# Kernel optimization log

Hardware: AMD Instinct MI355X
Metric: run time of the kernel (lower is better)

## Reference

```python
import jax, jax.numpy as jnp
import numpy as np

L, HID, NH, NKV, HD, INTER = 16, 960, 15, 5, 64, 2560
VOCAB, NV, NT, PRE, SD = 49152, 192, 48, 241, 32
THETA, EPS, B = 100000.0, 1e-5, 16
GROUPS = NH // NKV


def setup_inputs() -> dict:
    key = jax.random.key(0)
    ks = jax.random.split(key, 20)
    s = 0.02
    rn = lambda k, shp: jax.random.normal(k, shp, jnp.float32) * s
    return {
        'vision_features': jax.random.normal(ks[0], (B, NV, HID), jnp.float32),
        'lang_token_ids': jax.random.randint(ks[1], (B, NT), 0, VOCAB),
        'lang_mask': jnp.ones((B, NT), dtype=bool),
        'state': jax.random.normal(ks[2], (B, SD), jnp.float32),
        'embed': rn(ks[3], (VOCAB, HID)),
        'state_w': rn(ks[4], (SD, HID)),
        'state_b': jnp.zeros((HID,), jnp.float32),
        'Wq': rn(ks[5], (L, HID, NH * HD)),
        'Wk': rn(ks[6], (L, HID, NKV * HD)),
        'Wv': rn(ks[7], (L, HID, NKV * HD)),
        'Wo': rn(ks[8], (L, NH * HD, HID)),
        'Wg': rn(ks[9], (L, HID, INTER)),
        'Wu': rn(ks[10], (L, HID, INTER)),
        'Wd': rn(ks[11], (L, INTER, HID)),
        'ln1': jnp.ones((L, HID), jnp.float32),
        'ln2': jnp.ones((L, HID), jnp.float32),
    }


def _rms(x, w):
    var = jnp.mean(jnp.square(x), axis=-1, keepdims=True)
    return x * jax.lax.rsqrt(var + EPS) * w


def _rotate_half(x):
    h = x.shape[-1] // 2
    return jnp.concatenate([-x[..., h:], x[..., :h]], axis=-1)


def _rope_tables(position_ids):
    # position_ids: [B, S] -> cos/sin: [B, S, HD]
    inv_freq = 1.0 / (THETA ** (jnp.arange(0, HD, 2, dtype=jnp.float32) / HD))
    freqs = position_ids.astype(jnp.float32)[..., None] * inv_freq  # [B,S,HD/2]
    emb = jnp.concatenate([freqs, freqs], axis=-1)
    return jnp.cos(emb), jnp.sin(emb)


def _apply_rope(x, cos, sin):
    # x: [B,S,H,D]; cos/sin: [B,S,D]
    return x * cos[:, :, None, :] + _rotate_half(x) * sin[:, :, None, :]


def _attention(q, k, v, mask2d):
    # q: [B,S,NH,HD]; k,v: [B,S,NKV,HD]; mask2d: [B,S,S] bool (query i, key j)
    kx = jnp.repeat(k, GROUPS, axis=2)  # GQA expand -> [B,S,NH,HD]
    vx = jnp.repeat(v, GROUPS, axis=2)
    scores = jnp.einsum('bihd,bjhd->bhij', q, kx) * (HD ** -0.5)
    big_neg = jnp.finfo(jnp.float32).min
    scores = jnp.where(mask2d[:, None, :, :], scores, big_neg)
    probs = jax.nn.softmax(scores, axis=-1)
    out = jnp.einsum('bhij,bjhd->bihd', probs, vx)
    return out.reshape(q.shape[0], q.shape[1], NH * HD)


def reference(vision_features, lang_token_ids, lang_mask, state,
              embed, state_w, state_b, Wq, Wk, Wv, Wo, Wg, Wu, Wd, ln1, ln2):
    lang_emb = embed[lang_token_ids] * jnp.sqrt(jnp.float32(HID))  # [B,NT,HID]
    state_emb = (state @ state_w + state_b)[:, None, :]            # [B,1,HID]
    x = jnp.concatenate([vision_features, lang_emb, state_emb], axis=1)  # [B,PRE,HID]

    pad = jnp.concatenate([jnp.ones((B, NV), bool), lang_mask.astype(bool),
                           jnp.ones((B, 1), bool)], axis=1)  # [B,PRE]
    position_ids = jnp.clip(jnp.cumsum(pad.astype(jnp.int32), axis=1) - 1, 0, None)
    cos, sin = _rope_tables(position_ids)

    att_marks = jnp.zeros((PRE,), jnp.int32).at[NV + NT:].set(1)
    cum = jnp.cumsum(att_marks)
    att2d = cum[None, :] >= cum[:, None]  # [S_q, S_kv]: key cum <= query cum
    pad2d = pad[:, :, None] & pad[:, None, :]
    mask2d = att2d[None, :, :] & pad2d  # [B,S,S]

    def layer(x, w):
        h = _rms(x, w['ln1'])
        S = h.shape[1]
        q = (h @ w['Wq']).reshape(B, S, NH, HD)
        k = (h @ w['Wk']).reshape(B, S, NKV, HD)
        v = (h @ w['Wv']).reshape(B, S, NKV, HD)
        q = _apply_rope(q, cos, sin)
        k = _apply_rope(k, cos, sin)
        a = _attention(q, k, v, mask2d)
        x = x + a @ w['Wo']
        h2 = _rms(x, w['ln2'])
        m = (jax.nn.silu(h2 @ w['Wg']) * (h2 @ w['Wu'])) @ w['Wd']
        return x + m, (k, v)

    weights = {'Wq': Wq, 'Wk': Wk, 'Wv': Wv, 'Wo': Wo,
               'Wg': Wg, 'Wu': Wu, 'Wd': Wd, 'ln1': ln1, 'ln2': ln2}
    _, (keys, values) = jax.lax.scan(layer, x, weights)
    # keys/values: [L, B, PRE, NKV, HD]
    return keys, values
```

## Files before the change

### kernel.cpp

```cpp
#include <hip/hip_runtime.h>
#include <hip/hip_bf16.h>

namespace {

typedef __bf16 bf16_t;
typedef __bf16 bf16x8 __attribute__((ext_vector_type(8)));
typedef __bf16 bf16x4 __attribute__((ext_vector_type(4)));
typedef float f32x4 __attribute__((ext_vector_type(4)));

constexpr int kL     = 16;
constexpr int kHid   = 960;
constexpr int kNH    = 15;
constexpr int kNKV   = 5;
constexpr int kHD    = 64;
constexpr int kInter = 2560;
constexpr int kNV    = 192;
constexpr int kNT    = 48;
constexpr int kPre   = 241;
constexpr int kSD    = 32;
constexpr int kB     = 16;
constexpr int kTok   = kB * kPre;
constexpr int kTokP  = 3968;
constexpr int kQKV   = 1600;
constexpr float kEps = 1e-5f;
constexpr float kSqrtHid = 30.98386677f;

constexpr size_t kWoOff     = (size_t)1664 * 960;
constexpr size_t kWgOff     = kWoOff + (size_t)1024 * 960;
constexpr size_t kWuOff     = kWgOff + (size_t)2560 * 960;
constexpr size_t kWdOff     = kWuOff + (size_t)2560 * 960;
constexpr size_t kWPerLayer = kWdOff + (size_t)1024 * 2560;

__device__ __forceinline__ void gload16(const bf16_t* g, bf16_t* l) {
  __builtin_amdgcn_global_load_lds((const __attribute__((address_space(1))) void*)g,
                                   (__attribute__((address_space(3))) void*)l, 16, 0, 0);
}

__device__ __forceinline__ void xcd_tile(int& bx, int& by) {
  int nbx = gridDim.x;
  int nwg = nbx * gridDim.y;
  int orig = blockIdx.y * nbx + blockIdx.x;
  int q = nwg >> 3, r = nwg & 7;
  int xcd = orig & 7, pos = orig >> 3;
  int swz = (xcd < r) ? (xcd * (q + 1) + pos) : (r * (q + 1) + (xcd - r) * q + pos);
  bx = swz % nbx;
  by = swz / nbx;
}

__global__ void build_x_kernel(const float* __restrict__ vision,
                               const int*   __restrict__ tokens,
                               const float* __restrict__ state,
                               const float* __restrict__ embed,
                               const float* __restrict__ sw,
                               const float* __restrict__ sb,
                               float* __restrict__ x) {
  int idx = blockIdx.x * blockDim.x + threadIdx.x;
  if (idx >= kTok * kHid) return;
  int t = idx / kHid, c = idx - t * kHid;
  int b = t / kPre, s = t - b * kPre;
  float v;
  if (s < kNV) {
    v = vision[((size_t)b * kNV + s) * kHid + c];
  } else if (s < kNV + kNT) {
    int tok = tokens[b * kNT + (s - kNV)];
    v = embed[(size_t)tok * kHid + c] * kSqrtHid;
  } else {
    float acc = sb[c];
#pragma unroll
    for (int i = 0; i < kSD; ++i) acc += state[b * kSD + i] * sw[i * kHid + c];
    v = acc;
  }
  x[idx] = v;
}

__global__ void rope_table_kernel(float* __restrict__ cosT, float* __restrict__ sinT) {
  int idx = blockIdx.x * blockDim.x + threadIdx.x;
  if (idx >= kPre * 32) return;
  int s = idx >> 5, fi = idx & 31;
  float inv = __expf(-(2.0f * (float)fi / (float)kHD) * __logf(100000.0f));
  float fr = (float)s * inv;
  cosT[idx] = cosf(fr);
  sinT[idx] = sinf(fr);
}

__device__ void transpose_tile(const float* __restrict__ src, bf16_t* __restrict__ dst,
                               int K, int N, int tile) {
  __shared__ float ts[64][65];
  int ntn = N >> 6;
  int tk = tile / ntn, tn = tile - tk * ntn;
  int t = threadIdx.x;
  int r = t >> 2, c0 = (t & 3) << 4;
  const float* sp = src + (size_t)((tk << 6) + r) * N + (tn << 6) + c0;
  float4 a = ((const float4*)sp)[0];
  float4 b = ((const float4*)sp)[1];
  float4 c = ((const float4*)sp)[2];
  float4 d = ((const float4*)sp)[3];
  ts[r][c0 + 0] = a.x;  ts[r][c0 + 1] = a.y;  ts[r][c0 + 2] = a.z;  ts[r][c0 + 3] = a.w;
  ts[r][c0 + 4] = b.x;  ts[r][c0 + 5] = b.y;  ts[r][c0 + 6] = b.z;  ts[r][c0 + 7] = b.w;
  ts[r][c0 + 8] = c.x;  ts[r][c0 + 9] = c.y;  ts[r][c0 +10] = c.z;  ts[r][c0 +11] = c.w;
  ts[r][c0 +12] = d.x;  ts[r][c0 +13] = d.y;  ts[r][c0 +14] = d.z;  ts[r][c0 +15] = d.w;
  __syncthreads();
  bf16_t* dp = dst + (size_t)((tn << 6) + r) * K + (tk << 6) + c0;
  bf16x8 o0, o1;
#pragma unroll
  for (int i = 0; i < 8; ++i) o0[i] = (bf16_t)ts[c0 + i][r];
#pragma unroll
  for (int i = 0; i < 8; ++i) o1[i] = (bf16_t)ts[c0 + 8 + i][r];
  *(bf16x8*)dp = o0;
  *(bf16x8*)(dp + 8) = o1;
}

__global__ __launch_bounds__(256)
void wconv_kernel(const float* __restrict__ Wq, const float* __restrict__ Wk,
                  const float* __restrict__ Wv, const float* __restrict__ Wo,
                  const float* __restrict__ Wg, const float* __restrict__ Wu,
                  const float* __restrict__ Wd, bf16_t* __restrict__ wall) {
  int bid = blockIdx.x;
  int l = bid / 2400, t = bid - l * 2400;
  bf16_t* wl = wall + (size_t)l * kWPerLayer;
  if      (t < 225)  transpose_tile(Wq + (size_t)l * 921600, wl, 960, 960, t);
  else if (t < 300)  transpose_tile(Wk + (size_t)l * 307200, wl + (size_t)960 * 960, 960, 320, t - 225);
  else if (t < 375)  transpose_tile(Wv + (size_t)l * 307200, wl + (size_t)1280 * 960, 960, 320, t - 300);
  else if (t < 600)  transpose_tile(Wo + (size_t)l * 921600, wl + kWoOff, 960, 960, t - 375);
  else if (t < 1200) transpose_tile(Wg + (size_t)l * 2457600, wl + kWgOff, 960, 2560, t - 600);
  else if (t < 1800) transpose_tile(Wu + (size_t)l * 2457600, wl + kWuOff, 960, 2560, t - 1200);
  else               transpose_tile(Wd + (size_t)l * 2457600, wl + kWdOff, 2560, 960, t - 1800);
}

__global__ __launch_bounds__(256)
void rmsnorm_bf16_kernel(const float* __restrict__ x, const float* __restrict__ w,
                         bf16_t* __restrict__ h) {
  int wid = threadIdx.x >> 6, lane = threadIdx.x & 63;
  int t = blockIdx.x * 4 + wid;
  if (t >= kTok) return;
  const float* xr = x + (size_t)t * kHid;
  float4 v[4];
  float ss = 0.f;
#pragma unroll
  for (int i = 0; i < 4; ++i) {
    int j = lane + i * 64;
    v[i] = make_float4(0.f, 0.f, 0.f, 0.f);
    if (j < 240) v[i] = ((const float4*)xr)[j];
    ss += v[i].x * v[i].x + v[i].y * v[i].y + v[i].z * v[i].z + v[i].w * v[i].w;
  }
#pragma unroll
  for (int off = 32; off; off >>= 1) ss += __shfl_xor(ss, off);
  float scale = rsqrtf(ss * (1.f / (float)kHid) + kEps);
  bf16_t* hr = h + (size_t)t * kHid;
#pragma unroll
  for (int i = 0; i < 4; ++i) {
    int j = lane + i * 64;
    if (j < 240) {
      float4 wv = ((const float4*)w)[j];
      bf16x4 o;
      o[0] = (bf16_t)(v[i].x * scale * wv.x);
      o[1] = (bf16_t)(v[i].y * scale * wv.y);
      o[2] = (bf16_t)(v[i].z * scale * wv.z);
      o[3] = (bf16_t)(v[i].w * scale * wv.w);
      *(bf16x4*)&hr[j * 4] = o;
    }
  }
}


__global__ __launch_bounds__(256, 4)
void gemm_qkv_kernel(const bf16_t* __restrict__ A, const bf16_t* __restrict__ Bt,
                     bf16_t* __restrict__ qkv, float* __restrict__ outk,
                     float* __restrict__ outv,
                     const float* __restrict__ cosT, const float* __restrict__ sinT) {
  constexpr int K = kHid;
  constexpr int NT = K / 32;
  __shared__ alignas(16) bf16_t As[2][4096];
  __shared__ alignas(16) bf16_t Bs[2][2048];
  int tid = threadIdx.x;
  int bx, by;
  xcd_tile(bx, by);
  int m0 = by * 128, n0 = bx * 64;
  int lane = tid & 63, wid = tid >> 6;
  int wr = wid * 32;
  int r0 = tid >> 2, c0 = (tid & 3) * 8;
  int lr = lane & 15, lg = lane >> 4;

  const bf16_t* a0 = A + (size_t)(m0 + r0) * K + c0;
  const bf16_t* a1 = a0 + (size_t)64 * K;
  const bf16_t* b0 = Bt + (size_t)(n0 + r0) * K + c0;

  f32x4 acc[2][4];
#pragma unroll
  for (int m = 0; m < 2; ++m)
#pragma unroll
    for (int n = 0; n < 4; ++n) acc[m][n] = (f32x4){0.f, 0.f, 0.f, 0.f};

  int arow0 = (wr + lr) * 32 + lg * 8;
  int brow0 = lr * 32 + lg * 8;

  gload16(a0, &As[0][tid * 8]);
  gload16(a1, &As[0][2048 + tid * 8]);
  if (r0 < 64) gload16(b0, &Bs[0][tid * 8]);
  __syncthreads();

  int cur = 0;
  for (int t = 0; t < NT; ++t) {
    if (t + 1 < NT) {
      int k1 = (t + 1) * 32;
      gload16(a0 + k1, &As[cur ^ 1][tid * 8]);
      gload16(a1 + k1, &As[cur ^ 1][2048 + tid * 8]);
      gload16(b0 + k1, &Bs[cur ^ 1][tid * 8]);
    }
    bf16x8 af[2], bfr[4];
#pragma unroll
    for (int m = 0; m < 2; ++m) af[m] = *(const bf16x8*)&As[cur][arow0 + m * 16 * 32];
#pragma unroll
    for (int n = 0; n < 4; ++n) bfr[n] = *(const bf16x8*)&Bs[cur][brow0 + n * 16 * 32];
#pragma unroll
    for (int m = 0; m < 2; ++m)
#pragma unroll
      for (int n = 0; n < 4; ++n)
        acc[m][n] = __builtin_amdgcn_mfma_f32_16x16x32_bf16(af[m], bfr[n], acc[m][n], 0, 0, 0);
    __syncthreads();
    cur ^= 1;
  }

  int cbase = n0;
  int cr4 = lg * 4;
  if (cbase < 1280) {
    bool isQ = cbase < 960;
    float scale = isQ ? 0.125f : 1.0f;
#pragma unroll
    for (int m = 0; m < 2; ++m) {
      int row = m0 + wr + m * 16 + cr4;
#pragma unroll
      for (int r = 0; r < 4; ++r) {
        int rr = row + r;
        if (rr >= kTok) continue;
        int s = rr % kPre;
        bf16_t* qrow = qkv + (size_t)rr * kQKV + cbase;
        float* krow = outk + (size_t)rr * 320 + (cbase - 960);
#pragma unroll
        for (int n = 0; n < 2; ++n) {
          int d = n * 16 + lr;
          float c = cosT[s * 32 + d], sn = sinT[s * 32 + d];
          float lo = acc[m][n][r], hi = acc[m][n + 2][r];
          float y0 = lo * c - hi * sn;
          float y1 = hi * c + lo * sn;
          qrow[d]      = (bf16_t)(y0 * scale);
          qrow[d + 32] = (bf16_t)(y1 * scale);
          if (!isQ) { krow[d] = y0; krow[d + 32] = y1; }
        }
      }
    }
  } else {
#pragma unroll
    for (int m = 0; m < 2; ++m) {
      int row = m0 + wr + m * 16 + cr4;
#pragma unroll
      for (int r = 0; r < 4; ++r) {
        int rr = row + r;
        if (rr >= kTok) continue;
        bf16_t* qrow = qkv + (size_t)rr * kQKV + cbase;
        float* vrow = outv + (size_t)rr * 320 + (cbase - 1280);
#pragma unroll
        for (int n = 0; n < 4; ++n) {
          int d = n * 16 + lr;
          float v = acc[m][n][r];
          qrow[d] = (bf16_t)v;
          vrow[d] = v;
        }
      }
    }
  }
}

__global__ __launch_bounds__(256, 4)
void gemm_res_kernel(const bf16_t* __restrict__ A, const bf16_t* __restrict__ Bt,
                     const float* __restrict__ src, float* __restrict__ C,
                     int M, int N, int K) {
  __shared__ alignas(16) bf16_t As[2][4096];
  __shared__ alignas(16) bf16_t Bs[2][2048];
  int tid = threadIdx.x;
  int bx, by;
  xcd_tile(bx, by);
  int m0 = by * 128, n0 = bx * 64;
  int lane = tid & 63, wid = tid >> 6;
  int wr = wid * 32;
  int r0 = tid >> 2, c0 = (tid & 3) * 8;
  int lr = lane & 15, lg = lane >> 4;

  const bf16_t* a0 = A + (size_t)(m0 + r0) * K + c0;
  const bf16_t* a1 = a0 + (size_t)64 * K;
  const bf16_t* b0 = Bt + (size_t)(n0 + r0) * K + c0;

  f32x4 acc[2][4];
#pragma unroll
  for (int m = 0; m < 2; ++m)
#pragma unroll
    for (int n = 0; n < 4; ++n) acc[m][n] = (f32x4){0.f, 0.f, 0.f, 0.f};

  int arow0 = (wr + lr) * 32 + lg * 8;
  int brow0 = lr * 32 + lg * 8;

  gload16(a0, &As[0][tid * 8]);
  gload16(a1, &As[0][2048 + tid * 8]);
  gload16(b0, &Bs[0][tid * 8]);
  __syncthreads();

  int NT = K / 32;
  int cur = 0;
  for (int t = 0; t < NT; ++t) {
    if (t + 1 < NT) {
      int k1 = (t + 1) * 32;
      gload16(a0 + k1, &As[cur ^ 1][tid * 8]);
      gload16(a1 + k1, &As[cur ^ 1][2048 + tid * 8]);
      gload16(b0 + k1, &Bs[cur ^ 1][tid * 8]);
    }
    bf16x8 af[2], bfr[4];
#pragma unroll
    for (int m = 0; m < 2; ++m) af[m] = *(const bf16x8*)&As[cur][arow0 + m * 16 * 32];
#pragma unroll
    for (int n = 0; n < 4; ++n) bfr[n] = *(const bf16x8*)&Bs[cur][brow0 + n * 16 * 32];
#pragma unroll
    for (int m = 0; m < 2; ++m)
#pragma unroll
      for (int n = 0; n < 4; ++n)
        acc[m][n] = __builtin_amdgcn_mfma_f32_16x16x32_bf16(af[m], bfr[n], acc[m][n], 0, 0, 0);
    __syncthreads();
    cur ^= 1;
  }

  int cr4 = lg * 4;
#pragma unroll
  for (int m = 0; m < 2; ++m) {
    int row = m0 + wr + m * 16 + cr4;
#pragma unroll
    for (int n = 0; n < 4; ++n) {
      int col = n0 + n * 16 + lr;
#pragma unroll
      for (int r = 0; r < 4; ++r) {
        int rr = row + r;
        if (rr < M) {
          size_t off = (size_t)rr * N + col;
          C[off] = src[off] + acc[m][n][r];
        }
      }
    }
  }
}

__global__ __launch_bounds__(256)
void gemm_dual_kernel(const bf16_t* __restrict__ A, const bf16_t* __restrict__ Bg,
                      const bf16_t* __restrict__ Bu, bf16_t* __restrict__ act,
                      int M, int K) {
  __shared__ alignas(16) bf16_t As[2][4096];
  __shared__ alignas(16) bf16_t Gs[2][2048];
  __shared__ alignas(16) bf16_t Us[2][2048];
  int tid = threadIdx.x;
  int bx, by;
  xcd_tile(bx, by);
  int m0 = by * 128, n0 = bx * 64;
  int lane = tid & 63, wid = tid >> 6;
  int wr = wid * 32;
  int r0 = tid >> 2, c0 = (tid & 3) * 8;
  int lr = lane & 15, lg = lane >> 4;

  const bf16_t* a0 = A + (size_t)(m0 + r0) * K + c0;
  const bf16_t* a1 = a0 + (size_t)64 * K;
  const bf16_t* g0 = Bg + (size_t)(n0 + r0) * K + c0;
  const bf16_t* u0 = Bu + (size_t)(n0 + r0) * K + c0;

  f32x4 accg[2][4], accu[2][4];
#pragma unroll
  for (int m = 0; m < 2; ++m)
#pragma unroll
    for (int n = 0; n < 4; ++n) {
      accg[m][n] = (f32x4){0.f, 0.f, 0.f, 0.f};
      accu[m][n] = (f32x4){0.f, 0.f, 0.f, 0.f};
    }

  int arow0 = (wr + lr) * 32 + lg * 8;
  int brow0 = lr * 32 + lg * 8;

  gload16(a0, &As[0][tid * 8]);
  gload16(a1, &As[0][2048 + tid * 8]);
  gload16(g0, &Gs[0][tid * 8]);
  gload16(u0, &Us[0][tid * 8]);
  __syncthreads();

  int NT = K / 32;
  int cur = 0;
  for (int t = 0; t < NT; ++t) {
    if (t + 1 < NT) {
      int k1 = (t + 1) * 32;
      gload16(a0 + k1, &As[cur ^ 1][tid * 8]);
      gload16(a1 + k1, &As[cur ^ 1][2048 + tid * 8]);
      gload16(g0 + k1, &Gs[cur ^ 1][tid * 8]);
      gload16(u0 + k1, &Us[cur ^ 1][tid * 8]);
    }
    bf16x8 af[2], bfr[4];
#pragma unroll
    for (int m = 0; m < 2; ++m) af[m] = *(const bf16x8*)&As[cur][arow0 + m * 16 * 32];
#pragma unroll
    for (int n = 0; n < 4; ++n) bfr[n] = *(const bf16x8*)&Gs[cur][brow0 + n * 16 * 32];
#pragma unroll
    for (int m = 0; m < 2; ++m)
#pragma unroll
      for (int n = 0; n < 4; ++n)
        accg[m][n] = __builtin_amdgcn_mfma_f32_16x16x32_bf16(af[m], bfr[n], accg[m][n], 0, 0, 0);
#pragma unroll
    for (int n = 0; n < 4; ++n) bfr[n] = *(const bf16x8*)&Us[cur][brow0 + n * 16 * 32];
#pragma unroll
    for (int m = 0; m < 2; ++m)
#pragma unroll
      for (int n = 0; n < 4; ++n)
        accu[m][n] = __builtin_amdgcn_mfma_f32_16x16x32_bf16(af[m], bfr[n], accu[m][n], 0, 0, 0);
    __syncthreads();
    cur ^= 1;
  }

  int cr4 = lg * 4;
#pragma unroll
  for (int m = 0; m < 2; ++m) {
    int row = m0 + wr + m * 16 + cr4;
#pragma unroll
    for (int n = 0; n < 4; ++n) {
      int col = n0 + n * 16 + lr;
#pragma unroll
      for (int r = 0; r < 4; ++r) {
        int rr = row + r;
        if (rr < M) {
          float g = accg[m][n][r];
          float u = accu[m][n][r];
          float silu = g / (1.f + __expf(-g));
          act[(size_t)rr * kInter + col] = (bf16_t)(silu * u);
        }
      }
    }
  }
}

__global__ __launch_bounds__(256)
void attn_mfma_kernel(const bf16_t* __restrict__ qkv, bf16_t* __restrict__ aout) {
  int h = blockIdx.x, b = blockIdx.y;
  int kvh = h / 3;
  constexpr int LDK = 72;
  constexpr int LDV = 264;
  __shared__ alignas(16) bf16_t Ks[256 * LDK];
  __shared__ alignas(16) bf16_t Vt[64 * LDV];
  __shared__ alignas(16) bf16_t Ps[4][16 * LDV];
  const bf16_t* base = qkv + (size_t)b * kPre * kQKV;
  int tid = threadIdx.x;
  for (int i = tid; i < 2048; i += 256) {
    int j = i >> 3, c = (i & 7) * 8;
    bf16x8 k8, v8;
    if (j < kPre) {
      k8 = *(const bf16x8*)(base + (size_t)j * kQKV + 960 + kvh * 64 + c);
      v8 = *(const bf16x8*)(base + (size_t)j * kQKV + 1280 + kvh * 64 + c);
    } else {
#pragma unroll
      for (int e = 0; e < 8; ++e) { k8[e] = (bf16_t)0.f; v8[e] = (bf16_t)0.f; }
    }
    *(bf16x8*)&Ks[j * LDK + c] = k8;
#pragma unroll
    for (int e = 0; e < 8; ++e) Vt[(c + e) * LDV + j] = v8[e];
  }
  __syncthreads();
  int wid = tid >> 6, lane = tid & 63;
  int lr = lane & 15, lg = lane >> 4;
  bf16_t* myP = &Ps[wid][0];
  for (int qt = wid * 4; qt < wid * 4 + 4; ++qt) {
    int q0 = qt * 16;
    int qrow = q0 + lr; if (qrow > 240) qrow = 240;
    const bf16_t* qp = base + (size_t)qrow * kQKV + h * 64 + lg * 8;
    bf16x8 aq0 = *(const bf16x8*)qp;
    bf16x8 aq1 = *(const bf16x8*)(qp + 32);
    f32x4 sacc[16];
#pragma unroll
    for (int ct = 0; ct < 16; ++ct) sacc[ct] = (f32x4){0.f, 0.f, 0.f, 0.f};
#pragma unroll
    for (int ct = 0; ct < 16; ++ct) {
      int key = ct * 16 + lr;
      bf16x8 kb0 = *(const bf16x8*)&Ks[key * LDK + lg * 8];
      sacc[ct] = __builtin_amdgcn_mfma_f32_16x16x32_bf16(aq0, kb0, sacc[ct], 0, 0, 0);
      bf16x8 kb1 = *(const bf16x8*)&Ks[key * LDK + 32 + lg * 8];
      sacc[ct] = __builtin_amdgcn_mfma_f32_16x16x32_bf16(aq1, kb1, sacc[ct], 0, 0, 0);
    }
    float rmax[4] = {-1e30f, -1e30f, -1e30f, -1e30f};
#pragma unroll
    for (int ct = 0; ct < 16; ++ct) {
      int j = ct * 16 + lr;
#pragma unroll
      for (int r = 0; r < 4; ++r) {
        int q = q0 + lg * 4 + r;
        bool ok = (q < 240) ? (j < kPre) : (j == 240);
        float s = ok ? sacc[ct][r] : -1e30f;
        sacc[ct][r] = s;
        rmax[r] = fmaxf(rmax[r], s);
      }
    }
#pragma unroll
    for (int off = 8; off; off >>= 1) {
#pragma unroll
      for (int r = 0; r < 4; ++r) rmax[r] = fmaxf(rmax[r], __shfl_xor(rmax[r], off));
    }
    float rsum[4] = {0.f, 0.f, 0.f, 0.f};
#pragma unroll
    for (int ct = 0; ct < 16; ++ct) {
#pragma unroll
      for (int r = 0; r < 4; ++r) {
        float s = sacc[ct][r];
        float e = (s > -1e29f) ? __expf(s - rmax[r]) : 0.f;
        rsum[r] += e;
        myP[(lg * 4 + r) * LDV + ct * 16 + lr] = (bf16_t)e;
      }
    }
#pragma unroll
    for (int off = 8; off; off >>= 1) {
#pragma unroll
      for (int r = 0; r < 4; ++r) rsum[r] += __shfl_xor(rsum[r], off);
    }
    f32x4 oacc[4];
#pragma unroll
    for (int dt = 0; dt < 4; ++dt) oacc[dt] = (f32x4){0.f, 0.f, 0.f, 0.f};
#pragma unroll
    for (int ks = 0; ks < 8; ++ks) {
      bf16x8 pa = *(const bf16x8*)&myP[lr * LDV + ks * 32 + lg * 8];
#pragma unroll
      for (int dt = 0; dt < 4; ++dt) {
        bf16x8 vbf = *(const bf16x8*)&Vt[(dt * 16 + lr) * LDV + ks * 32 + lg * 8];
        oacc[dt] = __builtin_amdgcn_mfma_f32_16x16x32_bf16(pa, vbf, oacc[dt], 0, 0, 0);
      }
    }
    float linv[4];
#pragma unroll
    for (int r = 0; r < 4; ++r) linv[r] = 1.f / rsum[r];
#pragma unroll
    for (int dt = 0; dt < 4; ++dt) {
#pragma unroll
      for (int r = 0; r < 4; ++r) {
        int q = q0 + lg * 4 + r;
        if (q < kPre) {
          aout[((size_t)b * kPre + q) * kHid + h * 64 + dt * 16 + lr] =
              (bf16_t)(oacc[dt][r] * linv[r]);
        }
      }
    }
  }
}

}

extern "C" void kernel_launch(void* const* d_in, const int* in_sizes, int n_in,
                              void* d_out, int out_size, void* d_ws, size_t ws_size,
                              hipStream_t stream) {
  const float* vision = (const float*)d_in[0];
  const int*   tokens = (const int*)d_in[1];
  const float* state = (const float*)d_in[3];
  const float* embed = (const float*)d_in[4];
  const float* sw    = (const float*)d_in[5];
  const float* sb    = (const float*)d_in[6];
  const float* Wq    = (const float*)d_in[7];
  const float* Wk    = (const float*)d_in[8];
  const float* Wv    = (const float*)d_in[9];
  const float* Wo    = (const float*)d_in[10];
  const float* Wg    = (const float*)d_in[11];
  const float* Wu    = (const float*)d_in[12];
  const float* Wd    = (const float*)d_in[13];
  const float* ln1   = (const float*)d_in[14];
  const float* ln2   = (const float*)d_in[15];

  char* w = (char*)d_ws;
  float*  x      = (float*)w;   w += (size_t)kTok * kHid * 4;
  bf16_t* qkv    = (bf16_t*)w;  w += (size_t)kTok * kQKV * 2;
  bf16_t* h_bf   = (bf16_t*)w;  w += (size_t)kTokP * kHid * 2;
  bf16_t* a_bf   = (bf16_t*)w;  w += (size_t)kTokP * kHid * 2;
  bf16_t* act_bf = (bf16_t*)w;  w += (size_t)kTokP * kInter * 2;
  bf16_t* wall   = (bf16_t*)w;  w += kWPerLayer * kL * 2;
  float*  cosT   = (float*)w;   w += (size_t)kPre * 32 * 4;
  float*  sinT   = (float*)w;   w += (size_t)kPre * 32 * 4;

  float* out_k = (float*)d_out;
  float* out_v = out_k + (size_t)kL * kTok * 320;

  build_x_kernel<<<(kTok * kHid + 255) / 256, 256, 0, stream>>>(
      vision, tokens, state, embed, sw, sb, x);
  rope_table_kernel<<<(kPre * 32 + 255) / 256, 256, 0, stream>>>(cosT, sinT);
  wconv_kernel<<<2400 * kL, 256, 0, stream>>>(Wq, Wk, Wv, Wo, Wg, Wu, Wd, wall);

  for (int l = 0; l < kL; ++l) {
    bf16_t* wl = wall + (size_t)l * kWPerLayer;
    rmsnorm_bf16_kernel<<<(kTok + 3) / 4, 256, 0, stream>>>(x, ln1 + (size_t)l * kHid, h_bf);
    gemm_qkv_kernel<<<dim3(25, 31), 256, 0, stream>>>(
        h_bf, wl, qkv, out_k + (size_t)l * kTok * 320, out_v + (size_t)l * kTok * 320,
        cosT, sinT);
    attn_mfma_kernel<<<dim3(15, 16), 256, 0, stream>>>(qkv, a_bf);
    gemm_res_kernel<<<dim3(15, 31), 256, 0, stream>>>(
        a_bf, wl + kWoOff, x, x, kTok, kHid, kHid);
    rmsnorm_bf16_kernel<<<(kTok + 3) / 4, 256, 0, stream>>>(x, ln2 + (size_t)l * kHid, h_bf);
    gemm_dual_kernel<<<dim3(40, 31), 256, 0, stream>>>(
        h_bf, wl + kWgOff, wl + kWuOff, act_bf, kTok, kHid);
    gemm_res_kernel<<<dim3(15, 31), 256, 0, stream>>>(
        act_bf, wl + kWdOff, x, x, kTok, kHid, kInter);
  }
}
```

Measured before the change: 3.540 ms.

## Fold RMSNorm into GEMMs via per-row sum-of-squares and weight-folded ln

Removes both per-layer RMSNorm kernels. The ln weights are folded into the bf16 transposed Wq/Wk/Wv/Wg/Wu at conversion time. The residual GEMMs now also write a bf16 copy of x and atomically accumulate per-row sums of squares, and the consuming GEMMs apply the rsqrt row scale in their epilogues. This saves two launches and two full activation passes per layer, in exchange for atomics, extra bf16 stores, and unnormalized bf16 inputs, which changes rounding behaviour.

```diff
diff --git a/kernel.cpp b/kernel.cpp
--- a/kernel.cpp
+++ b/kernel.cpp
@@ -53,7 +53,7 @@
                                const float* __restrict__ embed,
                                const float* __restrict__ sw,
                                const float* __restrict__ sb,
-                               float* __restrict__ x) {
+                               float* __restrict__ x, bf16_t* __restrict__ xb) {
   int idx = blockIdx.x * blockDim.x + threadIdx.x;
   if (idx >= kTok * kHid) return;
   int t = idx / kHid, c = idx - t * kHid;
@@ -71,6 +71,23 @@
     v = acc;
   }
   x[idx] = v;
+  xb[idx] = (bf16_t)v;
+}
+
+__global__ __launch_bounds__(256)
+void rowssq_kernel(const float* __restrict__ x, float* __restrict__ ssq) {
+  int t = blockIdx.x;
+  int tid = threadIdx.x;
+  const float* xr = x + (size_t)t * kHid;
+  float4 v = make_float4(0.f, 0.f, 0.f, 0.f);
+  if (tid < 240) v = ((const float4*)xr)[tid];
+  float ss = v.x * v.x + v.y * v.y + v.z * v.z + v.w * v.w;
+#pragma unroll
+  for (int off = 32; off; off >>= 1) ss += __shfl_xor(ss, off);
+  __shared__ float part[4];
+  if ((tid & 63) == 0) part[tid >> 6] = ss;
+  __syncthreads();
+  if (tid == 0) ssq[t] = part[0] + part[1] + part[2] + part[3];
 }
 
 __global__ void rope_table_kernel(float* __restrict__ cosT, float* __restrict__ sinT) {
@@ -84,7 +101,7 @@
 }
 
 __device__ void transpose_tile(const float* __restrict__ src, bf16_t* __restrict__ dst,
-                               int K, int N, int tile) {
+                               const float* __restrict__ lnw, int K, int N, int tile) {
   __shared__ float ts[64][65];
   int ntn = N >> 6;
   int tk = tile / ntn, tn = tile - tk * ntn;
@@ -100,12 +117,15 @@
   ts[r][c0 + 8] = c.x;  ts[r][c0 + 9] = c.y;  ts[r][c0 +10] = c.z;  ts[r][c0 +11] = c.w;
   ts[r][c0 +12] = d.x;  ts[r][c0 +13] = d.y;  ts[r][c0 +14] = d.z;  ts[r][c0 +15] = d.w;
   __syncthreads();
+  float wv[16];
+#pragma unroll
+  for (int i = 0; i < 16; ++i) wv[i] = lnw ? lnw[(tk << 6) + c0 + i] : 1.f;
   bf16_t* dp = dst + (size_t)((tn << 6) + r) * K + (tk << 6) + c0;
   bf16x8 o0, o1;
 #pragma unroll
-  for (int i = 0; i < 8; ++i) o0[i] = (bf16_t)ts[c0 + i][r];
-#pragma unroll
-  for (int i = 0; i < 8; ++i) o1[i] = (bf16_t)ts[c0 + 8 + i][r];
+  for (int i = 0; i < 8; ++i) o0[i] = (bf16_t)(ts[c0 + i][r] * wv[i]);
+#pragma unroll
+  for (int i = 0; i < 8; ++i) o1[i] = (bf16_t)(ts[c0 + 8 + i][r] * wv[8 + i]);
   *(bf16x8*)dp = o0;
   *(bf16x8*)(dp + 8) = o1;
 }
@@ -114,57 +134,26 @@
 void wconv_kernel(const float* __restrict__ Wq, const float* __restrict__ Wk,
                   const float* __restrict__ Wv, const float* __restrict__ Wo,
                   const float* __restrict__ Wg, const float* __restrict__ Wu,
-                  const float* __restrict__ Wd, bf16_t* __restrict__ wall) {
+                  const float* __restrict__ Wd, const float* __restrict__ ln1,
+                  const float* __restrict__ ln2, bf16_t* __restrict__ wall) {
   int bid = blockIdx.x;
   int l = bid / 2400, t = bid - l * 2400;
   bf16_t* wl = wall + (size_t)l * kWPerLayer;
-  if      (t < 225)  transpose_tile(Wq + (size_t)l * 921600, wl, 960, 960, t);
-  else if (t < 300)  transpose_tile(Wk + (size_t)l * 307200, wl + (size_t)960 * 960, 960, 320, t - 225);
-  else if (t < 375)  transpose_tile(Wv + (size_t)l * 307200, wl + (size_t)1280 * 960, 960, 320, t - 300);
-  else if (t < 600)  transpose_tile(Wo + (size_t)l * 921600, wl + kWoOff, 960, 960, t - 375);
-  else if (t < 1200) transpose_tile(Wg + (size_t)l * 2457600, wl + kWgOff, 960, 2560, t - 600);
-  else if (t < 1800) transpose_tile(Wu + (size_t)l * 2457600, wl + kWuOff, 960, 2560, t - 1200);
-  else               transpose_tile(Wd + (size_t)l * 2457600, wl + kWdOff, 2560, 960, t - 1800);
-}
-
-__global__ __launch_bounds__(256)
-void rmsnorm_bf16_kernel(const float* __restrict__ x, const float* __restrict__ w,
-                         bf16_t* __restrict__ h) {
-  int wid = threadIdx.x >> 6, lane = threadIdx.x & 63;
-  int t = blockIdx.x * 4 + wid;
-  if (t >= kTok) return;
-  const float* xr = x + (size_t)t * kHid;
-  float4 v[4];
-  float ss = 0.f;
-#pragma unroll
-  for (int i = 0; i < 4; ++i) {
-    int j = lane + i * 64;
-    v[i] = make_float4(0.f, 0.f, 0.f, 0.f);
-    if (j < 240) v[i] = ((const float4*)xr)[j];
-    ss += v[i].x * v[i].x + v[i].y * v[i].y + v[i].z * v[i].z + v[i].w * v[i].w;
-  }
-#pragma unroll
-  for (int off = 32; off; off >>= 1) ss += __shfl_xor(ss, off);
-  float scale = rsqrtf(ss * (1.f / (float)kHid) + kEps);
-  bf16_t* hr = h + (size_t)t * kHid;
-#pragma unroll
-  for (int i = 0; i < 4; ++i) {
-    int j = lane + i * 64;
-    if (j < 240) {
-      float4 wv = ((const float4*)w)[j];
-      bf16x4 o;
-      o[0] = (bf16_t)(v[i].x * scale * wv.x);
-      o[1] = (bf16_t)(v[i].y * scale * wv.y);
-      o[2] = (bf16_t)(v[i].z * scale * wv.z);
-      o[3] = (bf16_t)(v[i].w * scale * wv.w);
-      *(bf16x4*)&hr[j * 4] = o;
-    }
-  }
+  const float* w1 = ln1 + (size_t)l * kHid;
+  const float* w2 = ln2 + (size_t)l * kHid;
+  if      (t < 225)  transpose_tile(Wq + (size_t)l * 921600, wl, w1, 960, 960, t);
+  else if (t < 300)  transpose_tile(Wk + (size_t)l * 307200, wl + (size_t)960 * 960, w1, 960, 320, t - 225);
+  else if (t < 375)  transpose_tile(Wv + (size_t)l * 307200, wl + (size_t)1280 * 960, w1, 960, 320, t - 300);
+  else if (t < 600)  transpose_tile(Wo + (size_t)l * 921600, wl + kWoOff, nullptr, 960, 960, t - 375);
+  else if (t < 1200) transpose_tile(Wg + (size_t)l * 2457600, wl + kWgOff, w2, 960, 2560, t - 600);
+  else if (t < 1800) transpose_tile(Wu + (size_t)l * 2457600, wl + kWuOff, w2, 960, 2560, t - 1200);
+  else               transpose_tile(Wd + (size_t)l * 2457600, wl + kWdOff, nullptr, 2560, 960, t - 1800);
 }
 
 
 __global__ __launch_bounds__(256, 4)
-void gemm_qkv_kernel(const bf16_t* __restrict__ A, const bf16_t* __restrict__ Bt,
+void gemm_qkv_kernel(const bf16_t* __restrict__ A, const float* __restrict__ ssq,
+                     const bf16_t* __restrict__ Bt,
                      bf16_t* __restrict__ qkv, float* __restrict__ outk,
                      float* __restrict__ outv,
                      const float* __restrict__ cosT, const float* __restrict__ sinT) {
@@ -196,7 +185,7 @@
 
   gload16(a0, &As[0][tid * 8]);
   gload16(a1, &As[0][2048 + tid * 8]);
-  if (r0 < 64) gload16(b0, &Bs[0][tid * 8]);
+  gload16(b0, &Bs[0][tid * 8]);
   __syncthreads();
 
   int cur = 0;
@@ -223,6 +212,13 @@
 
   int cbase = n0;
   int cr4 = lg * 4;
+  float srow[2][4];
+#pragma unroll
+  for (int m = 0; m < 2; ++m)
+#pragma unroll
+    for (int r = 0; r < 4; ++r)
+      srow[m][r] = rsqrtf(ssq[m0 + wr + m * 16 + cr4 + r] * (1.f / 960.f) + kEps);
+
   if (cbase < 1280) {
     bool isQ = cbase < 960;
     float scale = isQ ? 0.125f : 1.0f;
@@ -240,7 +236,8 @@
         for (int n = 0; n < 2; ++n) {
           int d = n * 16 + lr;
           float c = cosT[s * 32 + d], sn = sinT[s * 32 + d];
-          float lo = acc[m][n][r], hi = acc[m][n + 2][r];
+          float lo = acc[m][n][r] * srow[m][r];
+          float hi = acc[m][n + 2][r] * srow[m][r];
           float y0 = lo * c - hi * sn;
           float y1 = hi * c + lo * sn;
           qrow[d]      = (bf16_t)(y0 * scale);
@@ -262,7 +259,7 @@
 #pragma unroll
         for (int n = 0; n < 4; ++n) {
           int d = n * 16 + lr;
-          float v = acc[m][n][r];
+          float v = acc[m][n][r] * srow[m][r];
           qrow[d] = (bf16_t)v;
           vrow[d] = v;
         }
@@ -274,6 +271,7 @@
 __global__ __launch_bounds__(256, 4)
 void gemm_res_kernel(const bf16_t* __restrict__ A, const bf16_t* __restrict__ Bt,
                      const float* __restrict__ src, float* __restrict__ C,
+                     bf16_t* __restrict__ xb, float* __restrict__ ssq_out,
                      int M, int N, int K) {
   __shared__ alignas(16) bf16_t As[2][4096];
   __shared__ alignas(16) bf16_t Bs[2][2048];
@@ -328,6 +326,7 @@
   }
 
   int cr4 = lg * 4;
+  float ps[2][4] = {};
 #pragma unroll
   for (int m = 0; m < 2; ++m) {
     int row = m0 + wr + m * 16 + cr4;
@@ -339,17 +338,37 @@
         int rr = row + r;
         if (rr < M) {
           size_t off = (size_t)rr * N + col;
-          C[off] = src[off] + acc[m][n][r];
+          float val = src[off] + acc[m][n][r];
+          C[off] = val;
+          xb[off] = (bf16_t)val;
+          ps[m][r] += val * val;
         }
       }
     }
   }
+#pragma unroll
+  for (int m = 0; m < 2; ++m)
+#pragma unroll
+    for (int r = 0; r < 4; ++r) {
+#pragma unroll
+      for (int off = 8; off; off >>= 1) ps[m][r] += __shfl_xor(ps[m][r], off);
+    }
+  if (lr == 0) {
+#pragma unroll
+    for (int m = 0; m < 2; ++m) {
+#pragma unroll
+      for (int r = 0; r < 4; ++r) {
+        int rr = m0 + wr + m * 16 + cr4 + r;
+        if (rr < M) atomicAdd(&ssq_out[rr], ps[m][r]);
+      }
+    }
+  }
 }
 
 __global__ __launch_bounds__(256)
-void gemm_dual_kernel(const bf16_t* __restrict__ A, const bf16_t* __restrict__ Bg,
-                      const bf16_t* __restrict__ Bu, bf16_t* __restrict__ act,
-                      int M, int K) {
+void gemm_dual_kernel(const bf16_t* __restrict__ A, const float* __restrict__ ssq,
+                      const bf16_t* __restrict__ Bg, const bf16_t* __restrict__ Bu,
+                      bf16_t* __restrict__ act, int M, int K) {
   __shared__ alignas(16) bf16_t As[2][4096];
   __shared__ alignas(16) bf16_t Gs[2][2048];
   __shared__ alignas(16) bf16_t Us[2][2048];
@@ -417,6 +436,12 @@
   }
 
   int cr4 = lg * 4;
+  float srow[2][4];
+#pragma unroll
+  for (int m = 0; m < 2; ++m)
+#pragma unroll
+    for (int r = 0; r < 4; ++r)
+      srow[m][r] = rsqrtf(ssq[m0 + wr + m * 16 + cr4 + r] * (1.f / 960.f) + kEps);
 #pragma unroll
   for (int m = 0; m < 2; ++m) {
     int row = m0 + wr + m * 16 + cr4;
@@ -427,8 +452,8 @@
       for (int r = 0; r < 4; ++r) {
         int rr = row + r;
         if (rr < M) {
-          float g = accg[m][n][r];
-          float u = accu[m][n][r];
+          float g = accg[m][n][r] * srow[m][r];
+          float u = accu[m][n][r] * srow[m][r];
           float silu = g / (1.f + __expf(-g));
           act[(size_t)rr * kInter + col] = (bf16_t)(silu * u);
         }
@@ -568,36 +593,42 @@
   const float* ln2   = (const float*)d_in[15];
 
   char* w = (char*)d_ws;
-  float*  x      = (float*)w;   w += (size_t)kTok * kHid * 4;
+  float*  x      = (float*)w;   w += (size_t)kTokP * kHid * 4;
+  bf16_t* xb     = (bf16_t*)w;  w += (size_t)kTokP * kHid * 2;
   bf16_t* qkv    = (bf16_t*)w;  w += (size_t)kTok * kQKV * 2;
-  bf16_t* h_bf   = (bf16_t*)w;  w += (size_t)kTokP * kHid * 2;
   bf16_t* a_bf   = (bf16_t*)w;  w += (size_t)kTokP * kHid * 2;
   bf16_t* act_bf = (bf16_t*)w;  w += (size_t)kTokP * kInter * 2;
   bf16_t* wall   = (bf16_t*)w;  w += kWPerLayer * kL * 2;
   float*  cosT   = (float*)w;   w += (size_t)kPre * 32 * 4;
   float*  sinT   = (float*)w;   w += (size_t)kPre * 32 * 4;
+  float*  ssqA   = (float*)w;   w += (size_t)(kL + 1) * kTokP * 4;
+  float*  ssqB   = (float*)w;   w += (size_t)kL * kTokP * 4;
 
   float* out_k = (float*)d_out;
   float* out_v = out_k + (size_t)kL * kTok * 320;
 
+  hipMemsetAsync(ssqA, 0, (size_t)(2 * kL + 1) * kTokP * 4, stream);
+
   build_x_kernel<<<(kTok * kHid + 255) / 256, 256, 0, stream>>>(
-      vision, tokens, state, embed, sw, sb, x);
+      vision, tokens, state, embed, sw, sb, x, xb);
+  rowssq_kernel<<<kTok, 256, 0, stream>>>(x, ssqA);
   rope_table_kernel<<<(kPre * 32 + 255) / 256, 256, 0, stream>>>(cosT, sinT);
-  wconv_kernel<<<2400 * kL, 256, 0, stream>>>(Wq, Wk, Wv, Wo, Wg, Wu, Wd, wall);
+  wconv_kernel<<<2400 * kL, 256, 0, stream>>>(Wq, Wk, Wv, Wo, Wg, Wu, Wd, ln1, ln2, wall);
 
   for (int l = 0; l < kL; ++l) {
     bf16_t* wl = wall + (size_t)l * kWPerLayer;
-    rmsnorm_bf16_kernel<<<(kTok + 3) / 4, 256, 0, stream>>>(x, ln1 + (size_t)l * kHid, h_bf);
+    float* ssq1  = ssqA + (size_t)l * kTokP;
+    float* ssq1n = ssqA + (size_t)(l + 1) * kTokP;
+    float* ssq2  = ssqB + (size_t)l * kTokP;
     gemm_qkv_kernel<<<dim3(25, 31), 256, 0, stream>>>(
-        h_bf, wl, qkv, out_k + (size_t)l * kTok * 320, out_v + (size_t)l * kTok * 320,
-        cosT, sinT);
+        xb, ssq1, wl, qkv, out_k + (size_t)l * kTok * 320,
+        out_v + (size_t)l * kTok * 320, cosT, sinT);
     attn_mfma_kernel<<<dim3(15, 16), 256, 0, stream>>>(qkv, a_bf);
     gemm_res_kernel<<<dim3(15, 31), 256, 0, stream>>>(
-        a_bf, wl + kWoOff, x, x, kTok, kHid, kHid);
-    rmsnorm_bf16_kernel<<<(kTok + 3) / 4, 256, 0, stream>>>(x, ln2 + (size_t)l * kHid, h_bf);
+        a_bf, wl + kWoOff, x, x, xb, ssq2, kTok, kHid, kHid);
     gemm_dual_kernel<<<dim3(40, 31), 256, 0, stream>>>(
-        h_bf, wl + kWgOff, wl + kWuOff, act_bf, kTok, kHid);
+        xb, ssq2, wl + kWgOff, wl + kWuOff, act_bf, kTok, kHid);
     gemm_res_kernel<<<dim3(15, 31), 256, 0, stream>>>(
-        act_bf, wl + kWdOff, x, x, kTok, kHid, kInter);
-  }
-}
+        act_bf, wl + kWdOff, x, x, xb, ssq1n, kTok, kHid, kInter);
+  }
+}
```

Measured after the change: 3.494 ms. About the same (-1.3%).
